# Optimization experiments

Hardware: AMD Instinct MI355X
Metric: run time of the kernel (lower is better)

Reference implementation:

```python
import jax, jax.numpy as jnp
import numpy as np

DIM, NUM_HEADS, WINDOW = 1024, 16, 256
HEAD_DIM = DIM // NUM_HEADS
B, L = 2, 2048


def rotate_half(x):
    x1, x2 = jnp.split(x, 2, axis=-1)
    return jnp.concatenate([-x2, x1], axis=-1)


def setup_inputs() -> dict:
    key = jax.random.key(0)
    kx, kq, kk, kv, ko = jax.random.split(key, 5)
    x = jax.random.normal(kx, (B, L, DIM), dtype=jnp.float32)
    # realistic RoPE tables (L, head_dim)
    inv_freq = 1.0 / (10000.0 ** (np.arange(0, HEAD_DIM, 2, dtype=np.float32) / HEAD_DIM))
    ang = np.arange(L, dtype=np.float32)[:, None] * inv_freq[None, :]  # (L, hd/2)
    ang = np.concatenate([ang, ang], axis=-1)  # (L, hd)
    cos = jnp.asarray(np.cos(ang))
    sin = jnp.asarray(np.sin(ang))
    scale = 1.0 / np.sqrt(DIM)
    Wq = jax.random.normal(kq, (DIM, DIM), dtype=jnp.float32) * scale
    Wk = jax.random.normal(kk, (DIM, DIM), dtype=jnp.float32) * scale
    Wv = jax.random.normal(kv, (DIM, DIM), dtype=jnp.float32) * scale
    Wo = jax.random.normal(ko, (DIM, DIM), dtype=jnp.float32) * scale
    return {"x": x, "cos": cos, "sin": sin, "Wq": Wq, "Wk": Wk, "Wv": Wv, "Wo": Wo}


def reference(x, cos, sin, Wq, Wk, Wv, Wo):
    Bx, Lx, D = x.shape
    H, hd, w = NUM_HEADS, HEAD_DIM, WINDOW
    q = (x @ Wq.T).reshape(Bx, Lx, H, hd)
    k = (x @ Wk.T).reshape(Bx, Lx, H, hd)
    v = (x @ Wv.T).reshape(Bx, Lx, H, hd)
    c = cos[None, :, None, :]  # broadcast over batch, heads
    s = sin[None, :, None, :]
    q = q * c + rotate_half(q) * s
    k = k * c + rotate_half(k) * s
    # (B, H, L, hd)
    q = q.transpose(0, 2, 1, 3)
    k = k.transpose(0, 2, 1, 3)
    v = v.transpose(0, 2, 1, 3)
    i = jnp.arange(Lx)[:, None]
    j = jnp.arange(Lx)[None, :]
    # causal & within sliding window: i - w <= j <= i
    mask = (j <= i) & (j >= i - w)
    scores = jnp.einsum("bhqd,bhkd->bhqk", q, k) / jnp.sqrt(jnp.asarray(hd, x.dtype))
    scores = jnp.where(mask[None, None], scores, jnp.finfo(scores.dtype).min)
    attn = jax.nn.softmax(scores, axis=-1)
    out = jnp.einsum("bhqk,bhkd->bhqd", attn, v)
    out = out.transpose(0, 2, 1, 3).reshape(Bx, Lx, D)
    return out @ Wo.T
```

## Files before the change

kernel.cpp:

```cpp
#include <hip/hip_runtime.h>

#define DIM 1024
#define NH  16
#define HD  64
#define BB  2
#define LL  2048
#define WIN 256
#define MM  (BB * LL)
#define NQKV (3 * DIM)
#define SEG  (DIM * DIM)

typedef __bf16 bf16x8 __attribute__((ext_vector_type(8)));
typedef float  f32x4  __attribute__((ext_vector_type(4)));
typedef unsigned short u16x8 __attribute__((ext_vector_type(8)));

__device__ __forceinline__ unsigned short f2bf(float f) {
    union { float f; unsigned int i; } v; v.f = f;
    unsigned int r = v.i + 0x7fffu + ((v.i >> 16) & 1u);
    return (unsigned short)(r >> 16);
}
__device__ __forceinline__ bf16x8 load8bf(const unsigned short* p) {
    uint4 u = *reinterpret_cast<const uint4*>(p);
    return __builtin_bit_cast(bf16x8, u);
}
__device__ __forceinline__ void gll16(const void* g, void* l) {
    __builtin_amdgcn_global_load_lds(
        (const __attribute__((address_space(1))) unsigned int*)g,
        (__attribute__((address_space(3))) unsigned int*)l, 16, 0, 0);
}

__global__ __launch_bounds__(256) void convert_inputs(
    const float* __restrict__ x,
    const float* __restrict__ Wq, const float* __restrict__ Wk,
    const float* __restrict__ Wv, const float* __restrict__ Wo,
    unsigned short* __restrict__ xb,
    unsigned short* __restrict__ wqkv,
    unsigned short* __restrict__ wob)
{
    const int y = blockIdx.y;
    const size_t base = ((size_t)blockIdx.x * 256 + threadIdx.x) * 8;
    const float* src; unsigned short* dst;
    if (y < 4)       { src = x + (size_t)y * SEG;  dst = xb + (size_t)y * SEG; }
    else if (y == 4) { src = Wq; dst = wqkv; }
    else if (y == 5) { src = Wk; dst = wqkv + SEG; }
    else if (y == 6) { src = Wv; dst = wqkv + 2 * (size_t)SEG; }
    else             { src = Wo; dst = wob; }
    float4 a = ((const float4*)(src + base))[0];
    float4 b = ((const float4*)(src + base))[1];
    u16x8 r;
    r[0] = f2bf(a.x); r[1] = f2bf(a.y); r[2] = f2bf(a.z); r[3] = f2bf(a.w);
    r[4] = f2bf(b.x); r[5] = f2bf(b.y); r[6] = f2bf(b.z); r[7] = f2bf(b.w);
    *(u16x8*)(dst + base) = r;
}

__global__ __launch_bounds__(256, 4) void qkv_gemm(
    const unsigned short* __restrict__ xb,
    const unsigned short* __restrict__ wqkv,
    const float* __restrict__ cosb, const float* __restrict__ sinb,
    unsigned short* __restrict__ qws, unsigned short* __restrict__ kws,
    unsigned short* __restrict__ vT)
{
    __shared__ __align__(16) unsigned short smem[2 * 128 * 64];
    unsigned short* As = smem;
    unsigned short* Bs = smem + 128 * 64;
    const int t = threadIdx.x;
    const int lane = t & 63, w = t >> 6;
    const int wm = w >> 1, wn = w & 1;
    const int lr = lane & 15, quad = lane >> 4;

    const int id   = blockIdx.y * 24 + blockIdx.x;
    const int xcd  = id & 7, slot = id >> 3;
    const int bxn  = (xcd & 1) * 12 + (slot % 12);
    const int byn  = (xcd >> 1) * 8 + (slot / 12);
    const int n0 = bxn * 128, m0 = byn * 128;

    f32x4 acc[4][4];
    for (int i = 0; i < 4; i++) for (int j = 0; j < 4; j++) acc[i][j] = 0.0f;

    const int rsub = t >> 3;
    const int csw  = (t & 7) ^ (rsub & 7);
    const int sw7  = lr & 7;

    for (int k0 = 0; k0 < DIM; k0 += 64) {
        __syncthreads();
        #pragma unroll
        for (int p = 0; p < 4; p++) {
            const int row = p * 32 + rsub;
            gll16(xb   + (size_t)(m0 + row) * DIM + k0 + csw * 8,
                  &As[p * 2048 + t * 8]);
            gll16(wqkv + (size_t)(n0 + row) * DIM + k0 + csw * 8,
                  &Bs[p * 2048 + t * 8]);
        }
        __syncthreads();
        #pragma unroll
        for (int kk = 0; kk < 2; kk++) {
            bf16x8 af[4], bfr[4];
            #pragma unroll
            for (int mi = 0; mi < 4; mi++) {
                const int R = wm * 64 + mi * 16 + lr;
                af[mi] = load8bf(&As[R * 64 + (((kk * 4 + quad) ^ sw7) * 8)]);
            }
            #pragma unroll
            for (int ni = 0; ni < 4; ni++) {
                const int R = wn * 64 + ni * 16 + lr;
                bfr[ni] = load8bf(&Bs[R * 64 + (((kk * 4 + quad) ^ sw7) * 8)]);
            }
            #pragma unroll
            for (int mi = 0; mi < 4; mi++)
                #pragma unroll
                for (int ni = 0; ni < 4; ni++)
                    acc[mi][ni] = __builtin_amdgcn_mfma_f32_16x16x32_bf16(
                        af[mi], bfr[ni], acc[mi][ni], 0, 0, 0);
        }
    }

    const int ng = n0 + wn * 64;
    const int which = ng >> 10;
    const int h = (ng & (DIM - 1)) >> 6;

    if (which == 2) {
        __syncthreads();
        unsigned short* T = smem + w * 2048;
        const int token0 = m0 + wm * 64;
        const int b  = token0 >> 11;
        const int lg = (token0 & (LL - 1)) + (lane & 7) * 8;
        #pragma unroll
        for (int p = 0; p < 2; p++) {
            #pragma unroll
            for (int ni = 2 * p; ni < 2 * p + 2; ni++) {
                const int dl = (ni & 1) * 16 + lr;
                const int g4 = (dl & 7) << 2;
                #pragma unroll
                for (int mi = 0; mi < 4; mi++)
                    #pragma unroll
                    for (int reg = 0; reg < 4; reg++) {
                        const int l = mi * 16 + quad * 4 + reg;
                        const int cw = (l >> 1) ^ g4;
                        T[dl * 64 + cw * 2 + (l & 1)] = f2bf(acc[mi][ni][reg]);
                    }
            }
            #pragma unroll
            for (int s = 0; s < 4; s++) {
                const int dl = s * 8 + (lane >> 3);
                const int d  = p * 32 + dl;
                const int g4 = (dl & 7) << 2;
                const int pd = ((lane & 7) * 4) ^ g4;
                uint4 val = *(const uint4*)&T[dl * 64 + pd * 2];
                *(uint4*)&vT[((size_t)(b * NH + h) * HD + d) * LL + lg] = val;
            }
        }
    } else {
        unsigned short* dst = (which == 0) ? qws : kws;
        #pragma unroll
        for (int mi = 0; mi < 4; mi++) {
            #pragma unroll
            for (int reg = 0; reg < 4; reg++) {
                const int row = m0 + wm * 64 + mi * 16 + quad * 4 + reg;
                const int b = row >> 11, l = row & (LL - 1);
                #pragma unroll
                for (int ni = 0; ni < 4; ni++) {
                    const int d = ni * 16 + lr;
                    const float c = cosb[l * HD + d];
                    const float s = sinb[l * HD + d];
                    const float partner = (d < 32) ? -acc[mi][ni + 2][reg]
                                                   :  acc[mi][ni - 2][reg];
                    dst[((size_t)(b * NH + h) * LL + l) * HD + d] =
                        f2bf(acc[mi][ni][reg] * c + partner * s);
                }
            }
        }
    }
}

#define SW_SPAN 320
#define PSTR 40
__global__ __launch_bounds__(256, 3) void swa_attn(
    const unsigned short* __restrict__ qws,
    const unsigned short* __restrict__ kws,
    const unsigned short* __restrict__ vT,
    unsigned short* __restrict__ aout)
{
    __shared__ __align__(16) unsigned short Ks[SW_SPAN * 64];
    __shared__ __align__(16) unsigned short Pc[4][16][PSTR];

    const int t = threadIdx.x;
    const int lane = t & 63, w = t >> 6;
    const int qb = blockIdx.x, h = blockIdx.y, b = blockIdx.z;
    const int q0 = qb * 64;
    const int base_key = q0 - WIN;

    const int lr = lane & 15, quad = lane >> 4, ko = quad * 8;
    const size_t base = ((size_t)(b * NH + h)) * LL * HD;
    const unsigned short* Q  = qws + base;
    const unsigned short* K  = kws + base;
    const unsigned short* VT = vT + base;

    {
        const int rsub = t >> 3;
        const int csw  = (t & 7) ^ (rsub & 7);
        #pragma unroll
        for (int p = 0; p < 10; p++) {
            const int j = min(max(base_key + p * 32 + rsub, 0), LL - 1);
            gll16(K + (size_t)j * HD + csw * 8, &Ks[p * 2048 + t * 8]);
        }
    }
    const int i0 = q0 + w * 16;
    const int wkey = i0 - WIN;
    const bf16x8 qa0 = load8bf(Q + (size_t)(i0 + lr) * HD + ko);
    const bf16x8 qa1 = load8bf(Q + (size_t)(i0 + lr) * HD + 32 + ko);
    __syncthreads();

    float rowsum[4] = {0.f, 0.f, 0.f, 0.f};
    f32x4 o[4];
    #pragma unroll
    for (int nt = 0; nt < 4; nt++) o[nt] = 0.0f;

    #pragma unroll
    for (int kc = 0; kc < 9; kc++) {
        #pragma unroll
        for (int sub = 0; sub < 2; sub++) {
            const int kt = kc * 2 + sub;
            const int R = min(w * 16 + kt * 16 + lr, SW_SPAN - 1);
            const bf16x8 kb0 = load8bf(&Ks[R * 64 + ((quad       ^ (R & 7)) * 8)]);
            const bf16x8 kb1 = load8bf(&Ks[R * 64 + (((quad + 4) ^ (R & 7)) * 8)]);
            f32x4 s = 0.0f;
            s = __builtin_amdgcn_mfma_f32_16x16x32_bf16(qa0, kb0, s, 0, 0, 0);
            s = __builtin_amdgcn_mfma_f32_16x16x32_bf16(qa1, kb1, s, 0, 0, 0);
            #pragma unroll
            for (int reg = 0; reg < 4; reg++) {
                const int i = i0 + quad * 4 + reg;
                const int j = wkey + kt * 16 + lr;
                const bool valid = (j >= 0) && (j <= i) && (j >= i - WIN);
                const float e = valid ? __expf(s[reg] * 0.125f) : 0.0f;
                rowsum[reg] += e;
                Pc[w][quad * 4 + reg][sub * 16 + lr] = f2bf(e);
            }
        }
        const bf16x8 pa = load8bf(&Pc[w][lr][ko]);
        int kb = wkey + kc * 32 + ko;
        kb = min(max(kb, 0), LL - 8);
        bf16x8 bv[4];
        #pragma unroll
        for (int nt = 0; nt < 4; nt++)
            bv[nt] = load8bf(VT + (size_t)(nt * 16 + lr) * LL + kb);
        #pragma unroll
        for (int nt = 0; nt < 4; nt++)
            o[nt] = __builtin_amdgcn_mfma_f32_16x16x32_bf16(pa, bv[nt], o[nt], 0, 0, 0);
    }

    float inv[4];
    #pragma unroll
    for (int reg = 0; reg < 4; reg++) {
        float s = rowsum[reg];
        s += __shfl_xor(s, 1); s += __shfl_xor(s, 2);
        s += __shfl_xor(s, 4); s += __shfl_xor(s, 8);
        inv[reg] = 1.0f / s;
    }

    #pragma unroll
    for (int nt = 0; nt < 4; nt++) {
        #pragma unroll
        for (int reg = 0; reg < 4; reg++) {
            const int i = i0 + quad * 4 + reg;
            const int d = nt * 16 + lr;
            aout[((size_t)(b * LL + i)) * DIM + h * HD + d] =
                f2bf(o[nt][reg] * inv[reg]);
        }
    }
}

__global__ __launch_bounds__(256, 4) void out_gemm(
    const unsigned short* __restrict__ A,
    const unsigned short* __restrict__ Wob,
    float* __restrict__ out)
{
    __shared__ __align__(16) unsigned short smem[64 * 64 + 64 * 64];
    unsigned short* As = smem;
    unsigned short* Bs = smem + 64 * 64;
    const int t = threadIdx.x;
    const int lane = t & 63, w = t >> 6;
    const int wm = w >> 1, wn = w & 1;
    const int lr = lane & 15, quad = lane >> 4;

    const int id   = blockIdx.y * 16 + blockIdx.x;
    const int xcd  = id & 7, slot = id >> 3;
    const int bx   = (xcd & 1) * 8 + (slot & 7);
    const int by   = (xcd >> 1) * 16 + (slot >> 3);
    const int n0 = bx * 64, m0 = by * 64;

    f32x4 acc[2][2];
    for (int i = 0; i < 2; i++) for (int j = 0; j < 2; j++) acc[i][j] = 0.0f;

    const int rsub = t >> 3;
    const int csw  = (t & 7) ^ (rsub & 7);
    const int sw7  = lr & 7;

    for (int k0 = 0; k0 < DIM; k0 += 64) {
        __syncthreads();
        #pragma unroll
        for (int p = 0; p < 2; p++) {
            const int row = p * 32 + rsub;
            gll16(A   + (size_t)(m0 + row) * DIM + k0 + csw * 8,
                  &As[p * 2048 + t * 8]);
            gll16(Wob + (size_t)(n0 + row) * DIM + k0 + csw * 8,
                  &Bs[p * 2048 + t * 8]);
        }
        __syncthreads();
        #pragma unroll
        for (int kk = 0; kk < 2; kk++) {
            bf16x8 af[2], bfr[2];
            #pragma unroll
            for (int mi = 0; mi < 2; mi++) {
                const int R = wm * 32 + mi * 16 + lr;
                af[mi] = load8bf(&As[R * 64 + (((kk * 4 + quad) ^ sw7) * 8)]);
            }
            #pragma unroll
            for (int ni = 0; ni < 2; ni++) {
                const int R = wn * 32 + ni * 16 + lr;
                bfr[ni] = load8bf(&Bs[R * 64 + (((kk * 4 + quad) ^ sw7) * 8)]);
            }
            #pragma unroll
            for (int mi = 0; mi < 2; mi++)
                #pragma unroll
                for (int ni = 0; ni < 2; ni++)
                    acc[mi][ni] = __builtin_amdgcn_mfma_f32_16x16x32_bf16(
                        af[mi], bfr[ni], acc[mi][ni], 0, 0, 0);
        }
    }

    #pragma unroll
    for (int mi = 0; mi < 2; mi++) {
        #pragma unroll
        for (int reg = 0; reg < 4; reg++) {
            const int row = m0 + wm * 32 + mi * 16 + quad * 4 + reg;
            #pragma unroll
            for (int ni = 0; ni < 2; ni++) {
                const int col = n0 + wn * 32 + ni * 16 + lr;
                out[(size_t)row * DIM + col] = acc[mi][ni][reg];
            }
        }
    }
}

extern "C" void kernel_launch(void* const* d_in, const int* in_sizes, int n_in,
                              void* d_out, int out_size, void* d_ws, size_t ws_size,
                              hipStream_t stream)
{
    const float* x    = (const float*)d_in[0];
    const float* cosb = (const float*)d_in[1];
    const float* sinb = (const float*)d_in[2];
    const float* Wq   = (const float*)d_in[3];
    const float* Wk   = (const float*)d_in[4];
    const float* Wv   = (const float*)d_in[5];
    const float* Wo   = (const float*)d_in[6];
    float* out = (float*)d_out;

    unsigned short* xb   = (unsigned short*)d_ws;
    unsigned short* wqkv = xb + (size_t)MM * DIM;
    unsigned short* wob  = wqkv + (size_t)NQKV * DIM;
    unsigned short* qws  = wob + (size_t)DIM * DIM;
    unsigned short* kws  = qws + (size_t)BB * NH * LL * HD;
    unsigned short* vT   = kws + (size_t)BB * NH * LL * HD;
    unsigned short* aws  = xb;

    convert_inputs<<<dim3(SEG / (256 * 8), 8), 256, 0, stream>>>(
        x, Wq, Wk, Wv, Wo, xb, wqkv, wob);
    qkv_gemm<<<dim3(NQKV / 128, MM / 128), 256, 0, stream>>>(
        xb, wqkv, cosb, sinb, qws, kws, vT);
    swa_attn<<<dim3(LL / 64, NH, BB), 256, 0, stream>>>(qws, kws, vT, aws);
    out_gemm<<<dim3(DIM / 64, MM / 64), 256, 0, stream>>>(aws, wob, out);
}
```

Before: 159.8 us.

## Remap attention blocks per XCD, prefetch V tiles, skip masking on interior blocks

Block indices are remapped so that consecutive blocks dispatched to the same XCD share a head/batch, which improves L2 reuse of K/V. For query blocks past the window start, a fast path computes masks only on the boundary key tiles and skips the fully masked final tile, dropping per-element mask arithmetic. That path also software-pipelines the V-transpose global loads one chunk ahead of the PV MFMAs to hide load latency. The trade-off is extra registers for the prefetch buffers and duplicated code, which could lower occupancy.

```diff
diff --git a/kernel.cpp b/kernel.cpp
--- a/kernel.cpp
+++ b/kernel.cpp
@@ -185,7 +185,13 @@
 
     const int t = threadIdx.x;
     const int lane = t & 63, w = t >> 6;
-    const int qb = blockIdx.x, h = blockIdx.y, b = blockIdx.z;
+
+    const int id   = (blockIdx.z * 16 + blockIdx.y) * 32 + blockIdx.x;
+    const int xcd  = id & 7, slot = id >> 3;
+    const int hb   = xcd * 4 + (slot >> 5);
+    const int qb   = slot & 31;
+    const int h = hb & 15, b = hb >> 4;
+
     const int q0 = qb * 64;
     const int base_key = q0 - WIN;
 
@@ -215,37 +221,94 @@
     #pragma unroll
     for (int nt = 0; nt < 4; nt++) o[nt] = 0.0f;
 
-    #pragma unroll
-    for (int kc = 0; kc < 9; kc++) {
-        #pragma unroll
-        for (int sub = 0; sub < 2; sub++) {
-            const int kt = kc * 2 + sub;
-            const int R = min(w * 16 + kt * 16 + lr, SW_SPAN - 1);
-            const bf16x8 kb0 = load8bf(&Ks[R * 64 + ((quad       ^ (R & 7)) * 8)]);
-            const bf16x8 kb1 = load8bf(&Ks[R * 64 + (((quad + 4) ^ (R & 7)) * 8)]);
-            f32x4 s = 0.0f;
-            s = __builtin_amdgcn_mfma_f32_16x16x32_bf16(qa0, kb0, s, 0, 0, 0);
-            s = __builtin_amdgcn_mfma_f32_16x16x32_bf16(qa1, kb1, s, 0, 0, 0);
-            #pragma unroll
-            for (int reg = 0; reg < 4; reg++) {
-                const int i = i0 + quad * 4 + reg;
-                const int j = wkey + kt * 16 + lr;
-                const bool valid = (j >= 0) && (j <= i) && (j >= i - WIN);
-                const float e = valid ? __expf(s[reg] * 0.125f) : 0.0f;
-                rowsum[reg] += e;
-                Pc[w][quad * 4 + reg][sub * 16 + lr] = f2bf(e);
-            }
-        }
-        const bf16x8 pa = load8bf(&Pc[w][lr][ko]);
-        int kb = wkey + kc * 32 + ko;
-        kb = min(max(kb, 0), LL - 8);
+    if (q0 >= WIN) {
+        bool mlo[4], mhi[4];
+        #pragma unroll
+        for (int reg = 0; reg < 4; reg++) {
+            mlo[reg] = (lr >= quad * 4 + reg);
+            mhi[reg] = (lr <= quad * 4 + reg);
+        }
         bf16x8 bv[4];
         #pragma unroll
         for (int nt = 0; nt < 4; nt++)
-            bv[nt] = load8bf(VT + (size_t)(nt * 16 + lr) * LL + kb);
-        #pragma unroll
-        for (int nt = 0; nt < 4; nt++)
-            o[nt] = __builtin_amdgcn_mfma_f32_16x16x32_bf16(pa, bv[nt], o[nt], 0, 0, 0);
+            bv[nt] = load8bf(VT + (size_t)(nt * 16 + lr) * LL + wkey + ko);
+
+        #pragma unroll
+        for (int kc = 0; kc < 9; kc++) {
+            #pragma unroll
+            for (int sub = 0; sub < 2; sub++) {
+                const int kt = 2 * kc + sub;
+                if (kt > 16) {
+                    #pragma unroll
+                    for (int reg = 0; reg < 4; reg++)
+                        Pc[w][quad * 4 + reg][16 + lr] = 0;
+                } else {
+                    const int R = w * 16 + kt * 16 + lr;
+                    const bf16x8 kb0 = load8bf(&Ks[R * 64 + ((quad       ^ (R & 7)) * 8)]);
+                    const bf16x8 kb1 = load8bf(&Ks[R * 64 + (((quad + 4) ^ (R & 7)) * 8)]);
+                    f32x4 s = 0.0f;
+                    s = __builtin_amdgcn_mfma_f32_16x16x32_bf16(qa0, kb0, s, 0, 0, 0);
+                    s = __builtin_amdgcn_mfma_f32_16x16x32_bf16(qa1, kb1, s, 0, 0, 0);
+                    #pragma unroll
+                    for (int reg = 0; reg < 4; reg++) {
+                        float e = __expf(s[reg] * 0.125f);
+                        if (kt == 0)  e = mlo[reg] ? e : 0.0f;
+                        if (kt == 16) e = mhi[reg] ? e : 0.0f;
+                        rowsum[reg] += e;
+                        Pc[w][quad * 4 + reg][sub * 16 + lr] = f2bf(e);
+                    }
+                }
+            }
+            bf16x8 bvn[4];
+            if (kc < 8) {
+                int kb = wkey + (kc + 1) * 32 + ko;
+                kb = min(kb, LL - 8);
+                #pragma unroll
+                for (int nt = 0; nt < 4; nt++)
+                    bvn[nt] = load8bf(VT + (size_t)(nt * 16 + lr) * LL + kb);
+            }
+            const bf16x8 pa = load8bf(&Pc[w][lr][ko]);
+            #pragma unroll
+            for (int nt = 0; nt < 4; nt++)
+                o[nt] = __builtin_amdgcn_mfma_f32_16x16x32_bf16(pa, bv[nt], o[nt], 0, 0, 0);
+            if (kc < 8) {
+                #pragma unroll
+                for (int nt = 0; nt < 4; nt++) bv[nt] = bvn[nt];
+            }
+        }
+    } else {
+        #pragma unroll
+        for (int kc = 0; kc < 9; kc++) {
+            #pragma unroll
+            for (int sub = 0; sub < 2; sub++) {
+                const int kt = 2 * kc + sub;
+                const int R = min(w * 16 + kt * 16 + lr, SW_SPAN - 1);
+                const bf16x8 kb0 = load8bf(&Ks[R * 64 + ((quad       ^ (R & 7)) * 8)]);
+                const bf16x8 kb1 = load8bf(&Ks[R * 64 + (((quad + 4) ^ (R & 7)) * 8)]);
+                f32x4 s = 0.0f;
+                s = __builtin_amdgcn_mfma_f32_16x16x32_bf16(qa0, kb0, s, 0, 0, 0);
+                s = __builtin_amdgcn_mfma_f32_16x16x32_bf16(qa1, kb1, s, 0, 0, 0);
+                #pragma unroll
+                for (int reg = 0; reg < 4; reg++) {
+                    const int i = i0 + quad * 4 + reg;
+                    const int j = wkey + kt * 16 + lr;
+                    const bool valid = (j >= 0) && (j <= i) && (j >= i - WIN);
+                    const float e = valid ? __expf(s[reg] * 0.125f) : 0.0f;
+                    rowsum[reg] += e;
+                    Pc[w][quad * 4 + reg][sub * 16 + lr] = f2bf(e);
+                }
+            }
+            const bf16x8 pa = load8bf(&Pc[w][lr][ko]);
+            int kb = wkey + kc * 32 + ko;
+            kb = min(max(kb, 0), LL - 8);
+            bf16x8 bv[4];
+            #pragma unroll
+            for (int nt = 0; nt < 4; nt++)
+                bv[nt] = load8bf(VT + (size_t)(nt * 16 + lr) * LL + kb);
+            #pragma unroll
+            for (int nt = 0; nt < 4; nt++)
+                o[nt] = __builtin_amdgcn_mfma_f32_16x16x32_bf16(pa, bv[nt], o[nt], 0, 0, 0);
+        }
     }
 
     float inv[4];
```

Result: faster. 155.7 us (-2.6%).
